# Performance work log

Measured on AMD Instinct MI355X. Metric: run time of the kernel, lower is better.

## Reference

```python
import jax, jax.numpy as jnp
import numpy as np

N_NODES = 100000
N_HIGH = 20000
N_EDGES = 200000
D = 128
HEADS = 4
EPS = 1e-16


def setup_inputs() -> dict:
    key = jax.random.key(0)
    ks = jax.random.split(key, 9)
    s = 1.0 / np.sqrt(D)
    return {
        "n_features": jax.random.normal(ks[0], (N_NODES, D), jnp.float32),
        "W_src": jax.random.normal(ks[1], (D, HEADS * D), jnp.float32) * s,
        "W_dst": jax.random.normal(ks[2], (D, HEADS * D), jnp.float32) * s,
        "att_src": jax.random.normal(ks[3], (1, HEADS, D), jnp.float32) * s,
        "att_dst": jax.random.normal(ks[4], (1, HEADS, D), jnp.float32) * s,
        "W_high": jax.random.normal(ks[5], (D, D), jnp.float32) * s,
        "b_high": jnp.zeros((D,), jnp.float32),
        "src_idx": jax.random.randint(ks[6], (N_EDGES,), 0, N_NODES),
        "dst_idx": jax.random.randint(ks[7], (N_EDGES,), 0, N_HIGH),
    }


def reference(n_features, W_src, W_dst, att_src, att_dst, W_high, b_high, src_idx, dst_idx):
    # --- edge-wise gather of node features ---
    nn_features = n_features[src_idx]                      # [E, D]
    # --- scatter-mean to hyperedge features, gather back per edge ---
    seg_sum = jax.ops.segment_sum(nn_features, dst_idx, num_segments=N_HIGH)
    cnt = jax.ops.segment_sum(jnp.ones((src_idx.shape[0],), nn_features.dtype), dst_idx, num_segments=N_HIGH)
    h_mean = seg_sum / jnp.maximum(cnt, 1.0)[:, None]       # [H, D]
    h_high_e = h_mean[dst_idx]                              # [E, D]
    # --- per-edge multi-head projections ---
    E = src_idx.shape[0]
    h_node = (nn_features @ W_src).reshape(E, HEADS, D)     # [E, h, D]
    h_high = (h_high_e @ W_dst).reshape(E, HEADS, D)        # [E, h, D]
    # --- attention scores ---
    alpha_src = (h_high * att_src).sum(-1)                  # [E, h]
    alpha_dst = (h_node * att_dst).sum(-1)                  # [E, h]
    alpha = jax.nn.leaky_relu(alpha_src + alpha_dst, 0.2)
    # --- segment softmax over edges grouped by hyperedge id ---
    amax = jax.ops.segment_max(alpha, dst_idx, num_segments=N_HIGH)
    alpha = jnp.exp(alpha - amax[dst_idx])
    asum = jax.ops.segment_sum(alpha, dst_idx, num_segments=N_HIGH)
    alpha = alpha / (asum[dst_idx] + EPS)                   # [E, h]
    # --- weight, head-mean, scatter-sum aggregate ---
    h_node = (h_node * alpha[..., None]).mean(axis=1)       # [E, D]
    h_features = jax.ops.segment_sum(h_node, dst_idx, num_segments=N_HIGH)
    h_features = h_features @ W_high + b_high               # [H, D]
    return (h_features, alpha)
```

## Files before the change

kernel.cpp:

```cpp
#include <hip/hip_runtime.h>
#include <math.h>

#define N_NODES 100000
#define N_HIGH  20000
#define N_EDGES 200000
#define D       128
#define HEADS   4
#define EPSF    1e-16f

typedef __attribute__((ext_vector_type(8))) short bf16x8;
typedef __attribute__((ext_vector_type(4))) float f32x4;
typedef unsigned short ushort_t;
typedef unsigned int uint_t;

__device__ __forceinline__ ushort_t bf16_rn(float f) {
  uint_t u = __float_as_uint(f);
  u = u + 0x7FFFu + ((u >> 16) & 1u);
  return (ushort_t)(u >> 16);
}
__device__ __forceinline__ uint_t pack_bf2(float x, float y) {
  return (uint_t)bf16_rn(x) | ((uint_t)bf16_rn(y) << 16);
}
__device__ __forceinline__ float readlane_f(float v, int q) {
  return __uint_as_float(__builtin_amdgcn_readlane(__float_as_uint(v), q));
}

constexpr size_t OFF_VSRC = 0;
constexpr size_t OFF_VDST = OFF_VSRC + 512 * 4;
constexpr size_t OFF_P    = OFF_VDST + 512 * 4;
constexpr size_t OFF_ASRC = OFF_P    + 65536 * 4;
constexpr size_t OFF_ADST = OFF_ASRC + 400000 * 4;
constexpr size_t OFF_CNT  = OFF_ADST + 400000 * 4;
constexpr size_t OFF_OFFS = OFF_CNT  + 20000 * 4;
constexpr size_t OFF_FILL = OFF_OFFS + 20004 * 4;
constexpr size_t OFF_SORT = OFF_FILL + 20000 * 4;
constexpr size_t OFF_G    = OFF_SORT + 200000 * 8;
constexpr size_t OFF_NFB  = OFF_G    + 20000 * 512 * 2;

__global__ __launch_bounds__(256) void k_vp(
    const float* __restrict__ Wsrc, const float* __restrict__ Wdst,
    const float* __restrict__ att_src, const float* __restrict__ att_dst,
    const float* __restrict__ Whigh,
    float* __restrict__ v_src, float* __restrict__ v_dst,
    int* __restrict__ cnt, ushort_t* __restrict__ Pt) {
  __shared__ float red[128];
  if (blockIdx.x < 256) {
    int gid = blockIdx.x * 256 + threadIdx.x;
    if (gid < N_HIGH) cnt[gid] = 0;

    int W = blockIdx.x * 4 + (threadIdx.x >> 6);
    int lane = threadIdx.x & 63;
    int which = W >> 9;
    int idx = W & 511;
    int k = idx >> 2, h = idx & 3;
    const float* wrow = (which ? Wdst : Wsrc) + k * (HEADS * D) + h * D;
    const float* arow = (which ? att_src : att_dst) + h * D;
    float2 wv = ((const float2*)wrow)[lane];
    float2 av = ((const float2*)arow)[lane];
    float s = wv.x * av.x + wv.y * av.y;
#pragma unroll
    for (int o = 32; o; o >>= 1) s += __shfl_xor(s, o);
    if (lane == 0) {
      if (which) v_src[k * HEADS + h] = s;
      else       v_dst[k * HEADS + h] = s;
    }
  } else {
    int hk = blockIdx.x - 256;
    int h = hk >> 7, col = hk & 127;
    int d = threadIdx.x & 127, half = threadIdx.x >> 7;
    const float* ws = Wsrc + col * (HEADS * D) + h * D + half * 64;
    const float* wh = Whigh + (size_t)(half * 64) * D + d;
    float s = 0.f;
#pragma unroll 8
    for (int m = 0; m < 64; ++m) s += ws[m] * wh[(size_t)m * D];
    if (half) red[d] = s;
    __syncthreads();
    if (!half) {
      int kp = (col >> 1) * 8 + h * 2 + (col & 1);
      Pt[(size_t)d * 512 + kp] = bf16_rn(0.25f * (s + red[d]));
    }
  }
}

#define NP_BLOCKS 1563
#define H_BLOCKS  782
__global__ __launch_bounds__(256) void k_nodehist(
    const float* __restrict__ nf,
    const float* __restrict__ v_src, const float* __restrict__ v_dst,
    float4* __restrict__ a_srcn, float4* __restrict__ a_dstn,
    const int* __restrict__ dst, int* __restrict__ cnt,
    ushort_t* __restrict__ nfb) {
  __shared__ float nfT[128 * 65];
  __shared__ float4 vsf4[128];
  __shared__ float4 vdf4[128];
  __shared__ float part[8][4][64];
  int t = threadIdx.x;
  if (blockIdx.x >= NP_BLOCKS) {
    int e = (blockIdx.x - NP_BLOCKS) * 256 + t;
    if (e < N_EDGES) atomicAdd(&cnt[dst[e]], 1);
    return;
  }
  int n0 = blockIdx.x * 64;

  if (t < 128) vsf4[t] = ((const float4*)v_src)[t];
  else vdf4[t - 128] = ((const float4*)v_dst)[t - 128];

  const float4* nf4 = (const float4*)nf;
#pragma unroll
  for (int j = 0; j < 8; ++j) {
    int f4 = j * 256 + t;
    int r = f4 >> 5, c4 = f4 & 31;
    int n = n0 + r;
    if (n > N_NODES - 1) n = N_NODES - 1;
    float4 g = nf4[(size_t)n * 32 + c4];
    nfT[(c4 * 4 + 0) * 65 + r] = g.x;
    nfT[(c4 * 4 + 1) * 65 + r] = g.y;
    nfT[(c4 * 4 + 2) * 65 + r] = g.z;
    nfT[(c4 * 4 + 3) * 65 + r] = g.w;
    ushort4 hb;
    hb.x = bf16_rn(g.x); hb.y = bf16_rn(g.y);
    hb.z = bf16_rn(g.z); hb.w = bf16_rn(g.w);
    ((ushort4*)nfb)[(size_t)n * 32 + c4] = hb;
  }
  __syncthreads();

  int l = t & 63, w = t >> 6;
  float as[4] = {0.f, 0.f, 0.f, 0.f};
  float ad[4] = {0.f, 0.f, 0.f, 0.f};
#pragma unroll 8
  for (int kk = 0; kk < 32; ++kk) {
    int k = w * 32 + kk;
    float x = nfT[k * 65 + l];
    float4 s4 = vsf4[k];
    float4 d4 = vdf4[k];
    as[0] += x * s4.x; as[1] += x * s4.y; as[2] += x * s4.z; as[3] += x * s4.w;
    ad[0] += x * d4.x; ad[1] += x * d4.y; ad[2] += x * d4.z; ad[3] += x * d4.w;
  }
#pragma unroll
  for (int v = 0; v < 4; ++v) {
    part[v][w][l] = as[v];
    part[v + 4][w][l] = ad[v];
  }
  __syncthreads();

  if (t < 64) {
    int ll = t;
    if (n0 + ll < N_NODES) {
      float4 o;
      o.x = part[0][0][ll] + part[0][1][ll] + part[0][2][ll] + part[0][3][ll];
      o.y = part[1][0][ll] + part[1][1][ll] + part[1][2][ll] + part[1][3][ll];
      o.z = part[2][0][ll] + part[2][1][ll] + part[2][2][ll] + part[2][3][ll];
      o.w = part[3][0][ll] + part[3][1][ll] + part[3][2][ll] + part[3][3][ll];
      a_srcn[n0 + ll] = o;
    }
  } else if (t < 128) {
    int ll = t - 64;
    if (n0 + ll < N_NODES) {
      float4 o;
      o.x = part[4][0][ll] + part[4][1][ll] + part[4][2][ll] + part[4][3][ll];
      o.y = part[5][0][ll] + part[5][1][ll] + part[5][2][ll] + part[5][3][ll];
      o.z = part[6][0][ll] + part[6][1][ll] + part[6][2][ll] + part[6][3][ll];
      o.w = part[7][0][ll] + part[7][1][ll] + part[7][2][ll] + part[7][3][ll];
      a_dstn[n0 + ll] = o;
    }
  }
}

#define SCAN_PER 20
__global__ __launch_bounds__(1024) void k_scan(
    const int* __restrict__ cnt, int* __restrict__ offs) {
  __shared__ int sm[1024];
  int t = threadIdx.x;
  int base = t * SCAN_PER;
  int s = 0;
  for (int i = 0; i < SCAN_PER; ++i) {
    int idx = base + i;
    s += (idx < N_HIGH) ? cnt[idx] : 0;
  }
  sm[t] = s;
  __syncthreads();
  for (int o = 1; o < 1024; o <<= 1) {
    int v = (t >= o) ? sm[t - o] : 0;
    __syncthreads();
    if (t >= o) sm[t] += v;
    __syncthreads();
  }
  int run = (t > 0) ? sm[t - 1] : 0;
  for (int i = 0; i < SCAN_PER; ++i) {
    int idx = base + i;
    if (idx < N_HIGH) {
      offs[idx] = run;
      run += cnt[idx];
    }
  }
  if (t == 1023) offs[N_HIGH] = sm[1023];
}

__global__ void k_scatter(const int* __restrict__ dst, const int* __restrict__ src,
                          const int* __restrict__ offs,
                          int* __restrict__ cnt, int2* __restrict__ sorted) {
  int e = blockIdx.x * blockDim.x + threadIdx.x;
  if (e < N_EDGES) {
    int d = dst[e];
    int pos = offs[d] + (atomicSub(&cnt[d], 1) - 1);
    sorted[pos] = make_int2(e, src[e]);
  }
}

#define RS 520
__global__ __launch_bounds__(512) void k_mg(
    const ushort_t* __restrict__ nfb,
    const float4* __restrict__ a_srcn, const float4* __restrict__ a_dstn,
    const int* __restrict__ offs, const int2* __restrict__ sorted,
    const ushort_t* __restrict__ Pt, const float* __restrict__ b,
    float* __restrict__ alpha_out, float* __restrict__ out) {
  __shared__ ushort_t Gl[16 * RS];
  int t = threadIdx.x;
  int w = t >> 6, lane = t & 63;
  int j0 = blockIdx.x * 16;

  for (int jj = 0; jj < 2; ++jj) {
    int row = w * 2 + jj;
    int j = j0 + row;
    int o0 = offs[j], o1 = offs[j + 1];
    int deg = o1 - o0;
    float2 acc[4];
#pragma unroll
    for (int h = 0; h < 4; ++h) acc[h] = make_float2(0.f, 0.f);

    if (deg > 0 && deg <= 64) {
      bool act = lane < deg;
      int2 es = sorted[o0 + (act ? lane : 0)];
      int e = es.x, sreg = es.y;
      float4 as = make_float4(0.f, 0.f, 0.f, 0.f);
      float4 ad = make_float4(0.f, 0.f, 0.f, 0.f);
      if (act) { as = a_srcn[sreg]; ad = a_dstn[sreg]; }

      float s[4] = {as.x, as.y, as.z, as.w};
#pragma unroll
      for (int o = 32; o; o >>= 1)
#pragma unroll
        for (int h = 0; h < 4; ++h) s[h] += __shfl_xor(s[h], o);
      float invdeg = 1.0f / (float)deg;
      float p[4];
      p[0] = s[0] * invdeg + ad.x;
      p[1] = s[1] * invdeg + ad.y;
      p[2] = s[2] * invdeg + ad.z;
      p[3] = s[3] * invdeg + ad.w;
      float ex[4];
#pragma unroll
      for (int h = 0; h < 4; ++h) {
        p[h] = p[h] >= 0.f ? p[h] : 0.2f * p[h];
        ex[h] = act ? expf(p[h]) : 0.f;
      }
      float se[4] = {ex[0], ex[1], ex[2], ex[3]};
#pragma unroll
      for (int o = 32; o; o >>= 1)
#pragma unroll
        for (int h = 0; h < 4; ++h) se[h] += __shfl_xor(se[h], o);
      float al[4];
#pragma unroll
      for (int h = 0; h < 4; ++h) al[h] = ex[h] / (se[h] + EPSF);
      if (act)
        ((float4*)alpha_out)[e] = make_float4(al[0], al[1], al[2], al[3]);

#pragma unroll 2
      for (int q = 0; q < deg; ++q) {
        int sq = __builtin_amdgcn_readlane(sreg, q);
        float a0 = readlane_f(al[0], q);
        float a1 = readlane_f(al[1], q);
        float a2 = readlane_f(al[2], q);
        float a3 = readlane_f(al[3], q);
        uint_t xw = ((const uint_t*)nfb)[(size_t)sq * 64 + lane];
        float xx = __uint_as_float(xw << 16);
        float xy = __uint_as_float(xw & 0xFFFF0000u);
        acc[0].x += a0 * xx; acc[0].y += a0 * xy;
        acc[1].x += a1 * xx; acc[1].y += a1 * xy;
        acc[2].x += a2 * xx; acc[2].y += a2 * xy;
        acc[3].x += a3 * xx; acc[3].y += a3 * xy;
      }
    } else if (deg > 64) {
      float s[4] = {0.f, 0.f, 0.f, 0.f};
      for (int i = lane; i < deg; i += 64) {
        int2 es = sorted[o0 + i];
        float4 a = a_srcn[es.y];
        s[0] += a.x; s[1] += a.y; s[2] += a.z; s[3] += a.w;
      }
#pragma unroll
      for (int o = 32; o; o >>= 1)
#pragma unroll
        for (int h = 0; h < 4; ++h) s[h] += __shfl_xor(s[h], o);
      float ah[4];
      float invdeg = 1.0f / (float)deg;
#pragma unroll
      for (int h = 0; h < 4; ++h) ah[h] = s[h] * invdeg;

      float se[4] = {0.f, 0.f, 0.f, 0.f};
      for (int i = lane; i < deg; i += 64) {
        int2 es = sorted[o0 + i];
        float4 a = a_dstn[es.y];
        float p[4] = {ah[0] + a.x, ah[1] + a.y, ah[2] + a.z, ah[3] + a.w};
#pragma unroll
        for (int h = 0; h < 4; ++h) {
          float pp = p[h] >= 0.f ? p[h] : 0.2f * p[h];
          se[h] += expf(pp);
        }
      }
#pragma unroll
      for (int o = 32; o; o >>= 1)
#pragma unroll
        for (int h = 0; h < 4; ++h) se[h] += __shfl_xor(se[h], o);
      float inv[4];
#pragma unroll
      for (int h = 0; h < 4; ++h) inv[h] = 1.0f / (se[h] + EPSF);

      for (int c0 = 0; c0 < deg; c0 += 64) {
        int i = c0 + lane;
        float al[4] = {0.f, 0.f, 0.f, 0.f};
        int sreg = 0;
        if (i < deg) {
          int2 es = sorted[o0 + i];
          sreg = es.y;
          float4 a = a_dstn[sreg];
          float p[4] = {ah[0] + a.x, ah[1] + a.y, ah[2] + a.z, ah[3] + a.w};
#pragma unroll
          for (int h = 0; h < 4; ++h) {
            float pp = p[h] >= 0.f ? p[h] : 0.2f * p[h];
            al[h] = expf(pp) * inv[h];
          }
          ((float4*)alpha_out)[es.x] = make_float4(al[0], al[1], al[2], al[3]);
        }
        int cl = min(64, deg - c0);
#pragma unroll 2
        for (int q = 0; q < cl; ++q) {
          int sq = __builtin_amdgcn_readlane(sreg, q);
          float a0 = readlane_f(al[0], q);
          float a1 = readlane_f(al[1], q);
          float a2 = readlane_f(al[2], q);
          float a3 = readlane_f(al[3], q);
          uint_t xw = ((const uint_t*)nfb)[(size_t)sq * 64 + lane];
          float xx = __uint_as_float(xw << 16);
          float xy = __uint_as_float(xw & 0xFFFF0000u);
          acc[0].x += a0 * xx; acc[0].y += a0 * xy;
          acc[1].x += a1 * xx; acc[1].y += a1 * xy;
          acc[2].x += a2 * xx; acc[2].y += a2 * xy;
          acc[3].x += a3 * xx; acc[3].y += a3 * xy;
        }
      }
    }
    uint4 gw;
    gw.x = pack_bf2(acc[0].x, acc[0].y);
    gw.y = pack_bf2(acc[1].x, acc[1].y);
    gw.z = pack_bf2(acc[2].x, acc[2].y);
    gw.w = pack_bf2(acc[3].x, acc[3].y);
    *(uint4*)&Gl[row * RS + lane * 8] = gw;
  }
  __syncthreads();

  int lr = lane & 15, lg = lane >> 4;
  f32x4 c0 = (f32x4){0.f, 0.f, 0.f, 0.f};
  const ushort_t* Pa = Pt + (size_t)lr * 512 + lg * 8 + (size_t)w * 16 * 512;
#pragma unroll
  for (int kt = 0; kt < 16; ++kt) {
    bf16x8 a = *(const bf16x8*)&Gl[lr * RS + kt * 32 + lg * 8];
    bf16x8 b0 = *(const bf16x8*)(Pa + kt * 32);
    c0 = __builtin_amdgcn_mfma_f32_16x16x32_bf16(a, b0, c0, 0, 0, 0);
  }
  int col0 = w * 16 + lr;
  float bb0 = b[col0];
#pragma unroll
  for (int r = 0; r < 4; ++r) {
    int row = j0 + lg * 4 + r;
    out[(size_t)row * 128 + col0] = c0[r] + bb0;
  }
}

extern "C" void kernel_launch(void* const* d_in, const int* in_sizes, int n_in,
                              void* d_out, int out_size, void* d_ws, size_t ws_size,
                              hipStream_t stream) {
  const float* nf      = (const float*)d_in[0];
  const float* Wsrc    = (const float*)d_in[1];
  const float* Wdst    = (const float*)d_in[2];
  const float* att_src = (const float*)d_in[3];
  const float* att_dst = (const float*)d_in[4];
  const float* Whigh   = (const float*)d_in[5];
  const float* bhigh   = (const float*)d_in[6];
  const int*   src     = (const int*)d_in[7];
  const int*   dst     = (const int*)d_in[8];

  char* ws = (char*)d_ws;
  float*    v_src  = (float*)(ws + OFF_VSRC);
  float*    v_dst  = (float*)(ws + OFF_VDST);
  ushort_t* Pt     = (ushort_t*)(ws + OFF_P);
  float4*   a_srcn = (float4*)(ws + OFF_ASRC);
  float4*   a_dstn = (float4*)(ws + OFF_ADST);
  int*      cnt    = (int*)(ws + OFF_CNT);
  int*      offs   = (int*)(ws + OFF_OFFS);
  int2*     sorted = (int2*)(ws + OFF_SORT);
  ushort_t* nfb    = (ushort_t*)(ws + OFF_NFB);

  float* out_h     = (float*)d_out;
  float* out_alpha = (float*)d_out + (size_t)N_HIGH * D;

  k_vp<<<768, 256, 0, stream>>>(Wsrc, Wdst, att_src, att_dst, Whigh,
                                v_src, v_dst, cnt, Pt);
  k_nodehist<<<NP_BLOCKS + H_BLOCKS, 256, 0, stream>>>(
      nf, v_src, v_dst, a_srcn, a_dstn, dst, cnt, nfb);
  k_scan<<<1, 1024, 0, stream>>>(cnt, offs);
  k_scatter<<<(N_EDGES + 255) / 256, 256, 0, stream>>>(dst, src, offs, cnt, sorted);
  k_mg<<<N_HIGH / 16, 512, 0, stream>>>(nfb, a_srcn, a_dstn, offs, sorted,
                                        Pt, bhigh, out_alpha, out_h);
}
```

Measured before the change: 119.0 us.

## Interleave two hyperedge rows per wave and pack src/dst attention scalars

The per-wave loop over two hyperedges is replaced by processing both rows together. Their index loads, softmax reductions and gather-accumulate loops are interleaved so the two independent memory streams can overlap. The per-node src and dst attention float4s are also stored adjacently in one packed array, so each edge reads a single 32-byte region instead of two separate arrays. This raises register pressure, since two accumulator sets are live at once, and adds divergent branches when the two degrees differ.

```diff
diff --git a/kernel.cpp b/kernel.cpp
--- a/kernel.cpp
+++ b/kernel.cpp
@@ -28,9 +28,8 @@
 constexpr size_t OFF_VSRC = 0;
 constexpr size_t OFF_VDST = OFF_VSRC + 512 * 4;
 constexpr size_t OFF_P    = OFF_VDST + 512 * 4;
-constexpr size_t OFF_ASRC = OFF_P    + 65536 * 4;
-constexpr size_t OFF_ADST = OFF_ASRC + 400000 * 4;
-constexpr size_t OFF_CNT  = OFF_ADST + 400000 * 4;
+constexpr size_t OFF_APK  = OFF_P    + 65536 * 4;
+constexpr size_t OFF_CNT  = OFF_APK  + 800000 * 4;
 constexpr size_t OFF_OFFS = OFF_CNT  + 20000 * 4;
 constexpr size_t OFF_FILL = OFF_OFFS + 20004 * 4;
 constexpr size_t OFF_SORT = OFF_FILL + 20000 * 4;
@@ -87,7 +86,7 @@
 __global__ __launch_bounds__(256) void k_nodehist(
     const float* __restrict__ nf,
     const float* __restrict__ v_src, const float* __restrict__ v_dst,
-    float4* __restrict__ a_srcn, float4* __restrict__ a_dstn,
+    float4* __restrict__ a_pack,
     const int* __restrict__ dst, int* __restrict__ cnt,
     ushort_t* __restrict__ nfb) {
   __shared__ float nfT[128 * 65];
@@ -151,7 +150,7 @@
       o.y = part[1][0][ll] + part[1][1][ll] + part[1][2][ll] + part[1][3][ll];
       o.z = part[2][0][ll] + part[2][1][ll] + part[2][2][ll] + part[2][3][ll];
       o.w = part[3][0][ll] + part[3][1][ll] + part[3][2][ll] + part[3][3][ll];
-      a_srcn[n0 + ll] = o;
+      a_pack[(size_t)(n0 + ll) * 2] = o;
     }
   } else if (t < 128) {
     int ll = t - 64;
@@ -161,7 +160,7 @@
       o.y = part[5][0][ll] + part[5][1][ll] + part[5][2][ll] + part[5][3][ll];
       o.z = part[6][0][ll] + part[6][1][ll] + part[6][2][ll] + part[6][3][ll];
       o.w = part[7][0][ll] + part[7][1][ll] + part[7][2][ll] + part[7][3][ll];
-      a_dstn[n0 + ll] = o;
+      a_pack[(size_t)(n0 + ll) * 2 + 1] = o;
     }
   }
 }
@@ -210,7 +209,7 @@
 #define RS 520
 __global__ __launch_bounds__(512) void k_mg(
     const ushort_t* __restrict__ nfb,
-    const float4* __restrict__ a_srcn, const float4* __restrict__ a_dstn,
+    const float4* __restrict__ a_pack,
     const int* __restrict__ offs, const int2* __restrict__ sorted,
     const ushort_t* __restrict__ Pt, const float* __restrict__ b,
     float* __restrict__ alpha_out, float* __restrict__ out) {
@@ -218,72 +217,116 @@
   int t = threadIdx.x;
   int w = t >> 6, lane = t & 63;
   int j0 = blockIdx.x * 16;
-
-  for (int jj = 0; jj < 2; ++jj) {
-    int row = w * 2 + jj;
-    int j = j0 + row;
-    int o0 = offs[j], o1 = offs[j + 1];
-    int deg = o1 - o0;
-    float2 acc[4];
-#pragma unroll
-    for (int h = 0; h < 4; ++h) acc[h] = make_float2(0.f, 0.f);
-
-    if (deg > 0 && deg <= 64) {
-      bool act = lane < deg;
-      int2 es = sorted[o0 + (act ? lane : 0)];
-      int e = es.x, sreg = es.y;
-      float4 as = make_float4(0.f, 0.f, 0.f, 0.f);
-      float4 ad = make_float4(0.f, 0.f, 0.f, 0.f);
-      if (act) { as = a_srcn[sreg]; ad = a_dstn[sreg]; }
-
-      float s[4] = {as.x, as.y, as.z, as.w};
-#pragma unroll
-      for (int o = 32; o; o >>= 1)
-#pragma unroll
-        for (int h = 0; h < 4; ++h) s[h] += __shfl_xor(s[h], o);
-      float invdeg = 1.0f / (float)deg;
-      float p[4];
-      p[0] = s[0] * invdeg + ad.x;
-      p[1] = s[1] * invdeg + ad.y;
-      p[2] = s[2] * invdeg + ad.z;
-      p[3] = s[3] * invdeg + ad.w;
-      float ex[4];
+  int rowA = w * 2, rowB = rowA + 1;
+  int jA = j0 + rowA;
+  int oA0 = offs[jA], oA1 = offs[jA + 1], oB1 = offs[jA + 2];
+  int oB0 = oA1;
+  int degA = oA1 - oA0, degB = oB1 - oB0;
+
+  float2 accA[4], accB[4];
+#pragma unroll
+  for (int h = 0; h < 4; ++h) {
+    accA[h] = make_float2(0.f, 0.f);
+    accB[h] = make_float2(0.f, 0.f);
+  }
+
+  if (degA <= 64 && degB <= 64) {
+    bool actA = lane < degA, actB = lane < degB;
+    int idxA = min(oA0 + (actA ? lane : 0), N_EDGES - 1);
+    int idxB = min(oB0 + (actB ? lane : 0), N_EDGES - 1);
+    int2 esA = sorted[idxA];
+    int2 esB = sorted[idxB];
+    int eA = esA.x, srA = esA.y;
+    int eB = esB.x, srB = esB.y;
+    float4 z4 = make_float4(0.f, 0.f, 0.f, 0.f);
+    float4 asA = z4, adA = z4, asB = z4, adB = z4;
+    if (actA) { asA = a_pack[(size_t)srA * 2]; adA = a_pack[(size_t)srA * 2 + 1]; }
+    if (actB) { asB = a_pack[(size_t)srB * 2]; adB = a_pack[(size_t)srB * 2 + 1]; }
+
+    float sA[4] = {asA.x, asA.y, asA.z, asA.w};
+    float sB[4] = {asB.x, asB.y, asB.z, asB.w};
+#pragma unroll
+    for (int o = 32; o; o >>= 1)
 #pragma unroll
       for (int h = 0; h < 4; ++h) {
-        p[h] = p[h] >= 0.f ? p[h] : 0.2f * p[h];
-        ex[h] = act ? expf(p[h]) : 0.f;
-      }
-      float se[4] = {ex[0], ex[1], ex[2], ex[3]};
-#pragma unroll
-      for (int o = 32; o; o >>= 1)
-#pragma unroll
-        for (int h = 0; h < 4; ++h) se[h] += __shfl_xor(se[h], o);
-      float al[4];
-#pragma unroll
-      for (int h = 0; h < 4; ++h) al[h] = ex[h] / (se[h] + EPSF);
-      if (act)
-        ((float4*)alpha_out)[e] = make_float4(al[0], al[1], al[2], al[3]);
-
-#pragma unroll 2
-      for (int q = 0; q < deg; ++q) {
-        int sq = __builtin_amdgcn_readlane(sreg, q);
-        float a0 = readlane_f(al[0], q);
-        float a1 = readlane_f(al[1], q);
-        float a2 = readlane_f(al[2], q);
-        float a3 = readlane_f(al[3], q);
+        sA[h] += __shfl_xor(sA[h], o);
+        sB[h] += __shfl_xor(sB[h], o);
+      }
+    float invA = 1.0f / (float)max(degA, 1);
+    float invB = 1.0f / (float)max(degB, 1);
+    float adv[2][4] = {{adA.x, adA.y, adA.z, adA.w}, {adB.x, adB.y, adB.z, adB.w}};
+    float exA[4], exB[4];
+#pragma unroll
+    for (int h = 0; h < 4; ++h) {
+      float pA = sA[h] * invA + adv[0][h];
+      float pB = sB[h] * invB + adv[1][h];
+      pA = pA >= 0.f ? pA : 0.2f * pA;
+      pB = pB >= 0.f ? pB : 0.2f * pB;
+      exA[h] = actA ? expf(pA) : 0.f;
+      exB[h] = actB ? expf(pB) : 0.f;
+    }
+    float seA[4] = {exA[0], exA[1], exA[2], exA[3]};
+    float seB[4] = {exB[0], exB[1], exB[2], exB[3]};
+#pragma unroll
+    for (int o = 32; o; o >>= 1)
+#pragma unroll
+      for (int h = 0; h < 4; ++h) {
+        seA[h] += __shfl_xor(seA[h], o);
+        seB[h] += __shfl_xor(seB[h], o);
+      }
+    float alA[4], alB[4];
+#pragma unroll
+    for (int h = 0; h < 4; ++h) {
+      alA[h] = exA[h] / (seA[h] + EPSF);
+      alB[h] = exB[h] / (seB[h] + EPSF);
+    }
+    if (actA)
+      ((float4*)alpha_out)[eA] = make_float4(alA[0], alA[1], alA[2], alA[3]);
+    if (actB)
+      ((float4*)alpha_out)[eB] = make_float4(alB[0], alB[1], alB[2], alB[3]);
+
+    int dmax = max(degA, degB);
+#pragma unroll 4
+    for (int q = 0; q < dmax; ++q) {
+      if (q < degA) {
+        int sq = __builtin_amdgcn_readlane(srA, q);
+        float a0 = readlane_f(alA[0], q);
+        float a1 = readlane_f(alA[1], q);
+        float a2 = readlane_f(alA[2], q);
+        float a3 = readlane_f(alA[3], q);
         uint_t xw = ((const uint_t*)nfb)[(size_t)sq * 64 + lane];
         float xx = __uint_as_float(xw << 16);
         float xy = __uint_as_float(xw & 0xFFFF0000u);
-        acc[0].x += a0 * xx; acc[0].y += a0 * xy;
-        acc[1].x += a1 * xx; acc[1].y += a1 * xy;
-        acc[2].x += a2 * xx; acc[2].y += a2 * xy;
-        acc[3].x += a3 * xx; acc[3].y += a3 * xy;
-      }
-    } else if (deg > 64) {
+        accA[0].x += a0 * xx; accA[0].y += a0 * xy;
+        accA[1].x += a1 * xx; accA[1].y += a1 * xy;
+        accA[2].x += a2 * xx; accA[2].y += a2 * xy;
+        accA[3].x += a3 * xx; accA[3].y += a3 * xy;
+      }
+      if (q < degB) {
+        int sq = __builtin_amdgcn_readlane(srB, q);
+        float a0 = readlane_f(alB[0], q);
+        float a1 = readlane_f(alB[1], q);
+        float a2 = readlane_f(alB[2], q);
+        float a3 = readlane_f(alB[3], q);
+        uint_t xw = ((const uint_t*)nfb)[(size_t)sq * 64 + lane];
+        float xx = __uint_as_float(xw << 16);
+        float xy = __uint_as_float(xw & 0xFFFF0000u);
+        accB[0].x += a0 * xx; accB[0].y += a0 * xy;
+        accB[1].x += a1 * xx; accB[1].y += a1 * xy;
+        accB[2].x += a2 * xx; accB[2].y += a2 * xy;
+        accB[3].x += a3 * xx; accB[3].y += a3 * xy;
+      }
+    }
+  } else {
+    for (int pick = 0; pick < 2; ++pick) {
+      int o0 = pick ? oB0 : oA0;
+      int deg = pick ? degB : degA;
+      float2* acc = pick ? accB : accA;
+
       float s[4] = {0.f, 0.f, 0.f, 0.f};
       for (int i = lane; i < deg; i += 64) {
         int2 es = sorted[o0 + i];
-        float4 a = a_srcn[es.y];
+        float4 a = a_pack[(size_t)es.y * 2];
         s[0] += a.x; s[1] += a.y; s[2] += a.z; s[3] += a.w;
       }
 #pragma unroll
@@ -291,14 +334,14 @@
 #pragma unroll
         for (int h = 0; h < 4; ++h) s[h] += __shfl_xor(s[h], o);
       float ah[4];
-      float invdeg = 1.0f / (float)deg;
+      float invdeg = 1.0f / (float)max(deg, 1);
 #pragma unroll
       for (int h = 0; h < 4; ++h) ah[h] = s[h] * invdeg;
 
       float se[4] = {0.f, 0.f, 0.f, 0.f};
       for (int i = lane; i < deg; i += 64) {
         int2 es = sorted[o0 + i];
-        float4 a = a_dstn[es.y];
+        float4 a = a_pack[(size_t)es.y * 2 + 1];
         float p[4] = {ah[0] + a.x, ah[1] + a.y, ah[2] + a.z, ah[3] + a.w};
 #pragma unroll
         for (int h = 0; h < 4; ++h) {
@@ -321,7 +364,7 @@
         if (i < deg) {
           int2 es = sorted[o0 + i];
           sreg = es.y;
-          float4 a = a_dstn[sreg];
+          float4 a = a_pack[(size_t)sreg * 2 + 1];
           float p[4] = {ah[0] + a.x, ah[1] + a.y, ah[2] + a.z, ah[3] + a.w};
 #pragma unroll
           for (int h = 0; h < 4; ++h) {
@@ -348,13 +391,18 @@
         }
       }
     }
-    uint4 gw;
-    gw.x = pack_bf2(acc[0].x, acc[0].y);
-    gw.y = pack_bf2(acc[1].x, acc[1].y);
-    gw.z = pack_bf2(acc[2].x, acc[2].y);
-    gw.w = pack_bf2(acc[3].x, acc[3].y);
-    *(uint4*)&Gl[row * RS + lane * 8] = gw;
-  }
+  }
+  uint4 gwA, gwB;
+  gwA.x = pack_bf2(accA[0].x, accA[0].y);
+  gwA.y = pack_bf2(accA[1].x, accA[1].y);
+  gwA.z = pack_bf2(accA[2].x, accA[2].y);
+  gwA.w = pack_bf2(accA[3].x, accA[3].y);
+  gwB.x = pack_bf2(accB[0].x, accB[0].y);
+  gwB.y = pack_bf2(accB[1].x, accB[1].y);
+  gwB.z = pack_bf2(accB[2].x, accB[2].y);
+  gwB.w = pack_bf2(accB[3].x, accB[3].y);
+  *(uint4*)&Gl[rowA * RS + lane * 8] = gwA;
+  *(uint4*)&Gl[rowB * RS + lane * 8] = gwB;
   __syncthreads();
 
   int lr = lane & 15, lg = lane >> 4;
@@ -392,8 +440,7 @@
   float*    v_src  = (float*)(ws + OFF_VSRC);
   float*    v_dst  = (float*)(ws + OFF_VDST);
   ushort_t* Pt     = (ushort_t*)(ws + OFF_P);
-  float4*   a_srcn = (float4*)(ws + OFF_ASRC);
-  float4*   a_dstn = (float4*)(ws + OFF_ADST);
+  float4*   a_pack = (float4*)(ws + OFF_APK);
   int*      cnt    = (int*)(ws + OFF_CNT);
   int*      offs   = (int*)(ws + OFF_OFFS);
   int2*     sorted = (int2*)(ws + OFF_SORT);
@@ -405,9 +452,9 @@
   k_vp<<<768, 256, 0, stream>>>(Wsrc, Wdst, att_src, att_dst, Whigh,
                                 v_src, v_dst, cnt, Pt);
   k_nodehist<<<NP_BLOCKS + H_BLOCKS, 256, 0, stream>>>(
-      nf, v_src, v_dst, a_srcn, a_dstn, dst, cnt, nfb);
+      nf, v_src, v_dst, a_pack, dst, cnt, nfb);
   k_scan<<<1, 1024, 0, stream>>>(cnt, offs);
   k_scatter<<<(N_EDGES + 255) / 256, 256, 0, stream>>>(dst, src, offs, cnt, sorted);
-  k_mg<<<N_HIGH / 16, 512, 0, stream>>>(nfb, a_srcn, a_dstn, offs, sorted,
+  k_mg<<<N_HIGH / 16, 512, 0, stream>>>(nfb, a_pack, offs, sorted,
                                         Pt, bhigh, out_alpha, out_h);
 }
```

Measured after the change: 118.3 us. Within noise of the previous version (-0.6%).
